# Kernel tuning notes

Measured on AMD Instinct MI355X. Metric: run time of the kernel, lower is better.

## Reference

```python
import jax, jax.numpy as jnp
import numpy as np

LAMBDA_COORD = 5.0
LAMBDA_NOOBJ = 0.5


def _iou(box1, box2):
    # boxes: [..., 4] in (cx, cy, w, h) format. Matches YoloLoss.IOU:
    # returns 0 when x_right < x_left or y_bottom < y_top (strict),
    # else intersection / (area1 + area2 - intersection).
    x1, y1, w1, h1 = box1[..., 0], box1[..., 1], box1[..., 2], box1[..., 3]
    x2, y2, w2, h2 = box2[..., 0], box2[..., 1], box2[..., 2], box2[..., 3]
    x_left = jnp.maximum(x1 - w1 / 2, x2 - w2 / 2)
    y_top = jnp.maximum(y1 - h1 / 2, y2 - h2 / 2)
    x_right = jnp.minimum(x1 + w1 / 2, x2 + w2 / 2)
    y_bottom = jnp.minimum(y1 + h1 / 2, y2 + h2 / 2)
    valid = jnp.logical_and(x_right >= x_left, y_bottom >= y_top)
    inter = (x_right - x_left) * (y_bottom - y_top)
    union = w1 * h1 + w2 * h2 - inter
    safe_union = jnp.where(union == 0, 1.0, union)
    return jnp.where(valid, inter / safe_union, 0.0)


def setup_inputs() -> dict:
    key = jax.random.key(0)
    k1, k2 = jax.random.split(key)
    B, S, D = 16384, 7, 30  # D = 2*5 + 20
    y = jax.random.normal(k1, (B, S, S, D), dtype=jnp.float32)
    gt = jax.random.normal(k2, (B, S, S, D), dtype=jnp.float32)
    return {"y": y, "gt": gt}


def reference(y, gt):
    pred, target = y, gt
    batch_size = pred.shape[0]
    obj = (target[..., 4] > 0).astype(pred.dtype)      # [B,S,S]
    noobj = (target[..., 4] == 0).astype(pred.dtype)   # [B,S,S]

    # class loss (mask over class channels, indices 10:)
    class_loss = jnp.sum(obj[..., None] * (target[..., 10:] - pred[..., 10:]) ** 2)

    # no-object confidence loss (channel 4, mask before responsibility edits)
    conf_loss_no_obj = jnp.sum(noobj * (target[..., 4] - pred[..., 4]) ** 2)

    # per-cell IOU of target box vs both predicted boxes
    tbox = target[..., 0:4]
    iou1 = _iou(tbox, pred[..., 0:4])   # [B,S,S]
    iou2 = _iou(tbox, pred[..., 5:9])   # [B,S,S]

    # responsibility: keep box1 iff iou1 > iou2 (ties -> box2), as in the torch loop
    resp1 = (iou1 > iou2).astype(pred.dtype)
    m1 = obj * resp1          # box1 responsible mask
    m2 = obj * (1.0 - resp1)  # box2 responsible mask

    # object confidence loss: confidence target is the IOU of the responsible box
    conf_loss_obj = jnp.sum(m1 * (iou1 - pred[..., 4]) ** 2
                            + m2 * (iou2 - pred[..., 9]) ** 2)

    # xy loss (channels 0,1 / 5,6)
    xy_loss = jnp.sum(m1 * ((target[..., 0] - pred[..., 0]) ** 2
                            + (target[..., 1] - pred[..., 1]) ** 2)
                      + m2 * ((target[..., 0] - pred[..., 5]) ** 2
                              + (target[..., 1] - pred[..., 6]) ** 2))

    # wh loss (channels 2,3 / 7,8)
    wh_loss = jnp.sum(m1 * ((target[..., 2] - pred[..., 2]) ** 2
                            + (target[..., 3] - pred[..., 3]) ** 2)
                      + m2 * ((target[..., 2] - pred[..., 7]) ** 2
                              + (target[..., 3] - pred[..., 8]) ** 2))

    total = (LAMBDA_COORD * xy_loss + LAMBDA_COORD * wh_loss
             + conf_loss_obj + LAMBDA_NOOBJ * conf_loss_no_obj
             + class_loss) / batch_size
    return total
```

## Files before the change

### kernel.cpp

```cpp
#include <hip/hip_runtime.h>

#define LAMBDA_COORD 5.0f
#define LAMBDA_NOOBJ 0.5f
#define DD 30
#define BLOCK 64
#define CELLS 64
#define ITERS 4
#define F4_PER_CHUNK (CELLS * DD / 4)

typedef const __attribute__((address_space(1))) void* gas_ptr;
typedef __attribute__((address_space(3))) void* las_ptr;

__device__ __forceinline__ void glds16(const float4* g, void* l) {
    __builtin_amdgcn_global_load_lds((gas_ptr)g, (las_ptr)l, 16, 0, 0);
}

__device__ __forceinline__ float iou_t(float tx, float ty, float tw, float th,
                                       float px, float py, float pw, float ph) {
    float xl = fmaxf(tx - tw * 0.5f, px - pw * 0.5f);
    float yt = fmaxf(ty - th * 0.5f, py - ph * 0.5f);
    float xr = fminf(tx + tw * 0.5f, px + pw * 0.5f);
    float yb = fminf(ty + th * 0.5f, py + ph * 0.5f);
    bool valid = (xr >= xl) && (yb >= yt);
    float inter = (xr - xl) * (yb - yt);
    float uni = tw * th + pw * ph - inter;
    float safe = (uni == 0.0f) ? 1.0f : uni;
    return valid ? (inter / safe) : 0.0f;
}

__global__ __launch_bounds__(BLOCK) void yolo_loss_kernel(
    const float* __restrict__ pred, const float* __restrict__ targ,
    float* __restrict__ out) {
    __shared__ __align__(16) float sp[CELLS * DD];
    __shared__ __align__(16) float st[CELLS * DD];

    const int tid = threadIdx.x;
    float acc = 0.0f;

    for (int it = 0; it < ITERS; ++it) {
        const size_t chunk = (size_t)blockIdx.x * ITERS + it;
        const float4* gp = (const float4*)pred + chunk * F4_PER_CHUNK;
        const float4* gt = (const float4*)targ + chunk * F4_PER_CHUNK;

        __syncthreads();

#pragma unroll
        for (int j = 0; j < 7; ++j) {
            glds16(gp + j * 64 + tid, (char*)sp + j * 1024);
            glds16(gt + j * 64 + tid, (char*)st + j * 1024);
        }
        if (tid < 32) {
            glds16(gp + 448 + tid, (char*)sp + 7 * 1024);
            glds16(gt + 448 + tid, (char*)st + 7 * 1024);
        }
        __syncthreads();

        const float* p = &sp[tid * DD];
        const float* t = &st[tid * DD];

        float t4 = t[4];
        float obj = (t4 > 0.0f) ? 1.0f : 0.0f;
        float noobj = (t4 == 0.0f) ? 1.0f : 0.0f;

        float cls = 0.0f;
#pragma unroll
        for (int k = 10; k < 30; ++k) {
            float d = t[k] - p[k];
            cls += d * d;
        }
        cls *= obj;

        float d4 = t4 - p[4];
        float conf_noobj = noobj * d4 * d4;

        float tx = t[0], ty = t[1], tw = t[2], th = t[3];
        float iou1 = iou_t(tx, ty, tw, th, p[0], p[1], p[2], p[3]);
        float iou2 = iou_t(tx, ty, tw, th, p[5], p[6], p[7], p[8]);
        float resp1 = (iou1 > iou2) ? 1.0f : 0.0f;
        float m1 = obj * resp1;
        float m2 = obj * (1.0f - resp1);

        float e1 = iou1 - p[4];
        float e2 = iou2 - p[9];
        float conf_obj = m1 * e1 * e1 + m2 * e2 * e2;

        float dx1 = tx - p[0], dy1 = ty - p[1];
        float dx2 = tx - p[5], dy2 = ty - p[6];
        float xy = m1 * (dx1 * dx1 + dy1 * dy1) + m2 * (dx2 * dx2 + dy2 * dy2);

        float dw1 = tw - p[2], dh1 = th - p[3];
        float dw2 = tw - p[7], dh2 = th - p[8];
        float wh = m1 * (dw1 * dw1 + dh1 * dh1) + m2 * (dw2 * dw2 + dh2 * dh2);

        acc += LAMBDA_COORD * (xy + wh) + conf_obj + LAMBDA_NOOBJ * conf_noobj + cls;
    }

#pragma unroll
    for (int off = 32; off > 0; off >>= 1) acc += __shfl_down(acc, off);
    if (tid == 0) atomicAdd(out, acc * (1.0f / 16384.0f));
}

extern "C" void kernel_launch(void* const* d_in, const int* in_sizes, int n_in,
                              void* d_out, int out_size, void* d_ws, size_t ws_size,
                              hipStream_t stream) {
    const float* pred = (const float*)d_in[0];
    const float* targ = (const float*)d_in[1];
    float* out = (float*)d_out;

    hipMemsetAsync(out, 0, sizeof(float), stream);

    const int cells = in_sizes[0] / DD;
    const int grid = cells / (CELLS * ITERS);
    yolo_loss_kernel<<<grid, BLOCK, 0, stream>>>(pred, targ, out);
}
```

Before: 216.4 us.

## Replace async global-to-LDS loads with register-staged prefetch of next chunk

Drops the global_load_lds path and instead loads each chunk into registers, stores it to shared memory, then issues the global loads for the next chunk before computing on the current one. The aim is to overlap global memory latency with compute inside each single-wave block and to remove the two __syncthreads per iteration. In exchange it uses many more VGPRs (16 float4 staging registers), which can lower occupancy. It also relies on compiler barriers rather than real synchronization, which is only safe because the block is a single 64-thread wavefront.

```diff
diff --git a/kernel.cpp b/kernel.cpp
--- a/kernel.cpp
+++ b/kernel.cpp
@@ -6,14 +6,7 @@
 #define BLOCK 64
 #define CELLS 64
 #define ITERS 4
-#define F4_PER_CHUNK (CELLS * DD / 4)
-
-typedef const __attribute__((address_space(1))) void* gas_ptr;
-typedef __attribute__((address_space(3))) void* las_ptr;
-
-__device__ __forceinline__ void glds16(const float4* g, void* l) {
-    __builtin_amdgcn_global_load_lds((gas_ptr)g, (las_ptr)l, 16, 0, 0);
-}
+#define F4C (CELLS * DD / 4)
 
 __device__ __forceinline__ float iou_t(float tx, float ty, float tw, float th,
                                        float px, float py, float pw, float ph) {
@@ -35,25 +28,34 @@
     __shared__ __align__(16) float st[CELLS * DD];
 
     const int tid = threadIdx.x;
+    const float4* gp = (const float4*)pred + (size_t)blockIdx.x * (ITERS * F4C);
+    const float4* gt = (const float4*)targ + (size_t)blockIdx.x * (ITERS * F4C);
+    float4* lp = (float4*)sp;
+    float4* lt = (float4*)st;
+
+    float4 rp[8], rt[8];
+#pragma unroll
+    for (int j = 0; j < 7; ++j) { rp[j] = gp[j * 64 + tid]; rt[j] = gt[j * 64 + tid]; }
+    if (tid < 32) { rp[7] = gp[448 + tid]; rt[7] = gt[448 + tid]; }
+
     float acc = 0.0f;
 
+#pragma unroll
     for (int it = 0; it < ITERS; ++it) {
-        const size_t chunk = (size_t)blockIdx.x * ITERS + it;
-        const float4* gp = (const float4*)pred + chunk * F4_PER_CHUNK;
-        const float4* gt = (const float4*)targ + chunk * F4_PER_CHUNK;
+        asm volatile("" ::: "memory");
+#pragma unroll
+        for (int j = 0; j < 7; ++j) { lp[j * 64 + tid] = rp[j]; lt[j * 64 + tid] = rt[j]; }
+        if (tid < 32) { lp[448 + tid] = rp[7]; lt[448 + tid] = rt[7]; }
+        asm volatile("" ::: "memory");
 
-        __syncthreads();
-
+        if (it + 1 < ITERS) {
+            const float4* ngp = gp + (size_t)(it + 1) * F4C;
+            const float4* ngt = gt + (size_t)(it + 1) * F4C;
 #pragma unroll
-        for (int j = 0; j < 7; ++j) {
-            glds16(gp + j * 64 + tid, (char*)sp + j * 1024);
-            glds16(gt + j * 64 + tid, (char*)st + j * 1024);
+            for (int j = 0; j < 7; ++j) { rp[j] = ngp[j * 64 + tid]; rt[j] = ngt[j * 64 + tid]; }
+            if (tid < 32) { rp[7] = ngp[448 + tid]; rt[7] = ngt[448 + tid]; }
         }
-        if (tid < 32) {
-            glds16(gp + 448 + tid, (char*)sp + 7 * 1024);
-            glds16(gt + 448 + tid, (char*)st + 7 * 1024);
-        }
-        __syncthreads();
+        asm volatile("" ::: "memory");
 
         const float* p = &sp[tid * DD];
         const float* t = &st[tid * DD];
```

Result: slower. 236.4 us (+9.2%).
